# Kernel tuning notes

Hardware: AMD Instinct MI355X
Metric: run time of the kernel (lower is better)

Reference implementation:

```python
import jax, jax.numpy as jnp
import numpy as np

EPSILON = 10.0
N_ITERS = 10
TOL = 1e-06
N, DIM = 8192, 128


def setup_inputs() -> dict:
    key = jax.random.key(0)
    kx, ky = jax.random.split(key)
    x = jax.random.normal(kx, (N, DIM), dtype=jnp.float32)
    y = jax.random.normal(ky, (N, DIM), dtype=jnp.float32)
    return {"x": x, "y": y}


def _sinkhorn_plan(C):
    # uniform marginals, as in the torch module defaults
    n = C.shape[0]
    a = jnp.full((n,), 1.0 / n, dtype=C.dtype)
    b = a
    K = jnp.exp(-C / EPSILON)  # [n, n]
    u0 = jnp.ones((n,), dtype=C.dtype)
    v0 = jnp.ones((n,), dtype=C.dtype)

    def step(carry, _):
        u, v, done = carry
        u_new = a / (K @ v)
        v_new = b / (K.T @ u_new)
        # torch breaks AFTER applying the update, so the converging step is kept
        conv = jnp.linalg.norm(u_new - u) < TOL
        u = jnp.where(done, u, u_new)
        v = jnp.where(done, v, v_new)
        return (u, v, done | conv), None

    (u, v, _), _ = jax.lax.scan(step, (u0, v0, jnp.array(False)), None, length=N_ITERS)
    # diag(u) @ K @ diag(v) == u[:,None] * K * v[None,:] (no diag materialization)
    return u[:, None] * K * v[None, :]


def reference(x, y):
    # torch.cdist(x, y, p=2): pairwise L2 distances [n, n]
    x2 = jnp.sum(x * x, axis=1)
    y2 = jnp.sum(y * y, axis=1)
    d2 = x2[:, None] + y2[None, :] - 2.0 * (x @ y.T)
    C = jnp.sqrt(jnp.maximum(d2, 0.0))

    P = _sinkhorn_plan(C)
    transport_cost = jnp.sum(P * C)
    entropy = -jnp.sum(P * jnp.log(P + 1e-09))
    divergence = transport_cost + EPSILON * entropy
    return divergence, P
```

## Files before the change

kernel.cpp:

```cpp
#include <hip/hip_runtime.h>

#define N 8192
#define DIM 128
#define EPS 10.0f
#define AINV (1.0f / 8192.0f)
#define C1 (-0.14426950408889634f)
#define C1SQ (0.020813712f)

typedef __attribute__((ext_vector_type(8))) short short8;
typedef __attribute__((ext_vector_type(4))) float f32x4;

static __device__ __forceinline__ unsigned short f2bf(float f) {
  unsigned int b = __float_as_uint(f);
  unsigned int lsb = (b >> 16) & 1u;
  b += 0x7fffu + lsb;
  return (unsigned short)(b >> 16);
}

__global__ __launch_bounds__(256) void k_convert(const float* __restrict__ x, const float* __restrict__ y,
                                                 unsigned short* __restrict__ xb, unsigned short* __restrict__ yb,
                                                 float* __restrict__ x2, float* __restrict__ y2,
                                                 float* __restrict__ u, float* __restrict__ vpartB,
                                                 double* __restrict__ accs) {
  int r = blockIdx.x * 4 + (threadIdx.x >> 6);
  int l = threadIdx.x & 63;
  const float* src = (r < N) ? (x + (size_t)r * DIM) : (y + (size_t)(r - N) * DIM);
  float2 f = ((const float2*)src)[l];
  unsigned short* dst = (r < N) ? (xb + (size_t)r * DIM) : (yb + (size_t)(r - N) * DIM);
  ushort2 h; h.x = f2bf(f.x); h.y = f2bf(f.y);
  int di = (((l >> 2) ^ (r & 7)) << 2) | (l & 3);
  ((ushort2*)dst)[di] = h;
  float s = f.x * f.x + f.y * f.y;
#pragma unroll
  for (int off = 32; off >= 1; off >>= 1) s += __shfl_down(s, off);
  if (l == 0) { if (r < N) x2[r] = s; else y2[r - N] = s; }
  if (r < N) {
    if (l == 0) { u[r] = 1.f; vpartB[r] = AINV; }
    else if (l < 16) vpartB[(size_t)l * N + r] = 0.f;
  }
  if (r == 0 && l == 0) { accs[0] = 0.0; accs[1] = 0.0; }
}

__global__ __launch_bounds__(256, 3) void k_pass(const unsigned short* __restrict__ Ab,
                                                 const unsigned short* __restrict__ Bb,
                                                 const float* __restrict__ a2, const float* __restrict__ b2,
                                                 const float* __restrict__ wpart,
                                                 float* __restrict__ outpart,
                                                 float* __restrict__ u_arr,
                                                 int write_u) {
  __shared__ float wv_lds[1024];
  __shared__ float b2_lds[1024];
  const int jc = blockIdx.x;
  const int ic = blockIdx.y;
  const int i0 = ic * 128;
  const int tid = threadIdx.x;
  const int wid = tid >> 6, lane = tid & 63;
  const uint4* ag = (const uint4*)Ab + (size_t)i0 * 16;
  const uint4* bwin = (const uint4*)Bb + (size_t)jc * 1024 * 16;
  const int wr = (wid >> 1) * 64, wc = (wid & 1) * 32;
  const int lhi = lane >> 4, llo = lane & 15;
  short8 afr[4][4];
#pragma unroll
  for (int kk = 0; kk < 4; ++kk)
#pragma unroll
    for (int m = 0; m < 4; ++m) {
      int rx = wr + m * 16 + llo;
      afr[kk][m] = *(const short8*)(ag + rx * 16 + ((kk * 4 + lhi) ^ (rx & 7)));
    }
  float a2v[4][4], rsum[4][4];
#pragma unroll
  for (int m = 0; m < 4; ++m)
#pragma unroll
    for (int r = 0; r < 4; ++r) {
      a2v[m][r] = a2[i0 + wr + m * 16 + lhi * 4 + r] * C1SQ;
      rsum[m][r] = 0.f;
    }
  {
    const float4* wp4 = (const float4*)wpart;
    int w4 = jc * 256 + tid;
    float4 s4 = wp4[w4];
#pragma unroll
    for (int q = 1; q < 16; ++q) {
      float4 p = wp4[(size_t)q * 2048 + w4];
      s4.x += p.x; s4.y += p.y; s4.z += p.z; s4.w += p.w;
    }
    float4 wn;
    wn.x = AINV * __builtin_amdgcn_rcpf(s4.x);
    wn.y = AINV * __builtin_amdgcn_rcpf(s4.y);
    wn.z = AINV * __builtin_amdgcn_rcpf(s4.z);
    wn.w = AINV * __builtin_amdgcn_rcpf(s4.w);
    ((float4*)wv_lds)[tid] = wn;
    float4 b4 = ((const float4*)b2)[w4];
    b4.x *= C1SQ; b4.y *= C1SQ; b4.z *= C1SQ; b4.w *= C1SQ;
    ((float4*)b2_lds)[tid] = b4;
    if (write_u && ic == 0) ((float4*)u_arr)[w4] = wn;
  }
  __syncthreads();
  for (int sc = 0; sc < 16; ++sc) {
    float wv[2], b2v[2];
#pragma unroll
    for (int n = 0; n < 2; ++n) {
      int jl = sc * 64 + wc + n * 16 + llo;
      wv[n] = wv_lds[jl];
      b2v[n] = b2_lds[jl];
    }
    f32x4 acc[4][2];
    f32x4 zero = {0.f, 0.f, 0.f, 0.f};
#pragma unroll
    for (int m = 0; m < 4; ++m)
#pragma unroll
      for (int n = 0; n < 2; ++n) acc[m][n] = zero;
#pragma unroll
    for (int kk = 0; kk < 4; ++kk) {
      short8 bfr[2];
#pragma unroll
      for (int n = 0; n < 2; ++n) {
        int rw = sc * 64 + wc + n * 16 + llo;
        bfr[n] = *(const short8*)(bwin + (size_t)rw * 16 + ((kk * 4 + lhi) ^ (llo & 7)));
      }
#pragma unroll
      for (int m = 0; m < 4; ++m)
#pragma unroll
        for (int n = 0; n < 2; ++n)
          acc[m][n] = __builtin_amdgcn_mfma_f32_16x16x32_bf16(afr[kk][m], bfr[n], acc[m][n], 0, 0, 0);
    }
#pragma unroll
    for (int m = 0; m < 4; ++m)
#pragma unroll
      for (int n = 0; n < 2; ++n)
#pragma unroll
        for (int r = 0; r < 4; ++r) {
          float tt = fmaf(-2.f * C1SQ, acc[m][n][r], a2v[m][r] + b2v[n]);
          float ss = __builtin_amdgcn_sqrtf(fmaxf(tt, 0.f));
          rsum[m][r] = fmaf(__builtin_amdgcn_exp2f(-ss), wv[n], rsum[m][r]);
        }
  }
#pragma unroll
  for (int m = 0; m < 4; ++m)
#pragma unroll
    for (int r = 0; r < 4; ++r) {
      float s = rsum[m][r];
      s += __shfl_xor(s, 1);
      s += __shfl_xor(s, 2);
      s += __shfl_xor(s, 4);
      s += __shfl_xor(s, 8);
      rsum[m][r] = s;
    }
  if (llo == 0) {
    float* vp = outpart + (size_t)(jc * 2 + (wid & 1)) * N;
#pragma unroll
    for (int m = 0; m < 4; ++m)
#pragma unroll
      for (int r = 0; r < 4; ++r)
        vp[i0 + wr + m * 16 + lhi * 4 + r] = rsum[m][r];
  }
}

__global__ __launch_bounds__(256) void k_final(const unsigned short* __restrict__ xb,
                                               const unsigned short* __restrict__ yb,
                                               const float* __restrict__ x2, const float* __restrict__ y2,
                                               const float* __restrict__ u, const float* __restrict__ vpartB,
                                               float* __restrict__ D, double* __restrict__ accs) {
  __shared__ float vv_lds[128];
  __shared__ double r0[256], r1[256];
  const int bid = blockIdx.x;
  const int iy = (bid & 7) + ((bid >> 9) << 3);
  const int jx = (bid >> 3) & 63;
  const int i0 = iy * 128;
  const int j0 = jx * 128;
  const int tid = threadIdx.x;
  const uint4* xg = (const uint4*)xb + (size_t)i0 * 16;
  const uint4* yg = (const uint4*)yb + (size_t)j0 * 16;
  if (tid < 32) {
    const float4* vp4 = (const float4*)vpartB;
    int w4 = (j0 >> 2) + tid;
    float4 s4 = vp4[w4];
#pragma unroll
    for (int q = 1; q < 16; ++q) {
      float4 p = vp4[(size_t)q * 2048 + w4];
      s4.x += p.x; s4.y += p.y; s4.z += p.z; s4.w += p.w;
    }
    float4 vn;
    vn.x = AINV * __builtin_amdgcn_rcpf(s4.x);
    vn.y = AINV * __builtin_amdgcn_rcpf(s4.y);
    vn.z = AINV * __builtin_amdgcn_rcpf(s4.z);
    vn.w = AINV * __builtin_amdgcn_rcpf(s4.w);
    ((float4*)vv_lds)[tid] = vn;
  }
  __syncthreads();
  const int wid = tid >> 6, lane = tid & 63;
  const int wr = (wid >> 1) * 64, wc = (wid & 1) * 64;
  const int lhi = lane >> 4, llo = lane & 15;
  float x2v[4][4], uvv[4][4], y2v[4], vv[4];
#pragma unroll
  for (int m = 0; m < 4; ++m)
#pragma unroll
    for (int r = 0; r < 4; ++r) {
      int i = i0 + wr + m * 16 + lhi * 4 + r;
      x2v[m][r] = x2[i];
      uvv[m][r] = u[i];
    }
#pragma unroll
  for (int n = 0; n < 4; ++n) {
    int j = j0 + wc + n * 16 + llo;
    y2v[n] = y2[j];
    vv[n] = vv_lds[wc + n * 16 + llo];
  }
  f32x4 acc[4][4];
  f32x4 zero = {0.f, 0.f, 0.f, 0.f};
#pragma unroll
  for (int m = 0; m < 4; ++m)
#pragma unroll
    for (int n = 0; n < 4; ++n) acc[m][n] = zero;
#pragma unroll
  for (int kk = 0; kk < 4; ++kk) {
    short8 af[4], bfr[4];
#pragma unroll
    for (int m = 0; m < 4; ++m) {
      int rx = wr + m * 16 + llo;
      af[m] = *(const short8*)(xg + rx * 16 + ((kk * 4 + lhi) ^ (rx & 7)));
      int ry = wc + m * 16 + llo;
      bfr[m] = *(const short8*)(yg + ry * 16 + ((kk * 4 + lhi) ^ (ry & 7)));
    }
#pragma unroll
    for (int m = 0; m < 4; ++m)
#pragma unroll
      for (int n = 0; n < 4; ++n)
        acc[m][n] = __builtin_amdgcn_mfma_f32_16x16x32_bf16(af[m], bfr[n], acc[m][n], 0, 0, 0);
  }
  float lc = 0.f, le = 0.f;
#pragma unroll
  for (int m = 0; m < 4; ++m) {
#pragma unroll
    for (int n = 0; n < 4; ++n) {
#pragma unroll
      for (int r = 0; r < 4; ++r) {
        int i = i0 + wr + m * 16 + lhi * 4 + r;
        int j = j0 + wc + n * 16 + llo;
        float d2 = fmaf(-2.f, acc[m][n][r], x2v[m][r] + y2v[n]);
        float c = __builtin_amdgcn_sqrtf(fmaxf(d2, 0.f));
        float k = __builtin_amdgcn_exp2f(c * C1);
        float p = uvv[m][r] * k * vv[n];
        D[1 + (size_t)i * N + j] = p;
        lc = fmaf(p, c, lc);
        le = fmaf(p, __logf(p + 1e-9f), le);
      }
    }
  }
  r0[tid] = (double)lc;
  r1[tid] = (double)le;
  __syncthreads();
  for (int s = 128; s > 0; s >>= 1) {
    if (tid < s) {
      r0[tid] += r0[tid + s];
      r1[tid] += r1[tid + s];
    }
    __syncthreads();
  }
  if (tid == 0) {
    atomicAdd(&accs[0], r0[0]);
    atomicAdd(&accs[1], r1[0]);
  }
}

__global__ void k_write_div(float* D, const double* accs) {
  if (threadIdx.x == 0 && blockIdx.x == 0)
    D[0] = (float)(accs[0] - (double)EPS * accs[1]);
}

extern "C" void kernel_launch(void* const* d_in, const int* in_sizes, int n_in,
                              void* d_out, int out_size, void* d_ws, size_t ws_size,
                              hipStream_t stream) {
  const float* x = (const float*)d_in[0];
  const float* y = (const float*)d_in[1];
  float* D = (float*)d_out;
  char* w = (char*)d_ws;
  unsigned short* xb = (unsigned short*)w;
  unsigned short* yb = (unsigned short*)(w + 2097152);
  float* fb = (float*)(w + 4194304);
  float* x2 = fb;
  float* y2 = fb + 8192;
  float* u = fb + 16384;
  float* vpartA = fb + 24576;
  float* vpartB = vpartA + 16 * N;
  double* accs = (double*)(vpartB + 16 * N);

  k_convert<<<4096, 256, 0, stream>>>(x, y, xb, yb, x2, y2, u, vpartB, accs);
  k_pass<<<dim3(8, 64), 256, 0, stream>>>(xb, yb, x2, y2, vpartB, vpartA, u, 0);
  k_pass<<<dim3(8, 64), 256, 0, stream>>>(yb, xb, y2, x2, vpartA, vpartB, u, 0);
  k_pass<<<dim3(8, 64), 256, 0, stream>>>(xb, yb, x2, y2, vpartB, vpartA, u, 0);
  k_pass<<<dim3(8, 64), 256, 0, stream>>>(yb, xb, y2, x2, vpartA, vpartB, u, 1);
  k_final<<<4096, 256, 0, stream>>>(xb, yb, x2, y2, u, vpartB, D, accs);
  k_write_div<<<1, 64, 0, stream>>>(D, accs);
}
```

Baseline: 254.0 us.

## Store bf16 operands in MFMA fragment order and restructure final plan kernel

The convert kernel now writes bf16 x/y in a fragment-major layout (16-row groups, 64 lanes per k-chunk), so every MFMA operand load in the pass and final kernels becomes one contiguous 16-byte-per-lane read without XOR swizzle arithmetic. The final kernel is reorganised so each block handles 16 rows across half the columns, keeping the A fragments resident and streaming B. It also writes D in row-contiguous 16-wide segments. The v reconstruction from partial sums is moved into a small separate kernel that packs v with y2, which adds one extra launch.

```diff
diff --git a/kernel.cpp b/kernel.cpp
--- a/kernel.cpp
+++ b/kernel.cpp
@@ -26,10 +26,11 @@
   int l = threadIdx.x & 63;
   const float* src = (r < N) ? (x + (size_t)r * DIM) : (y + (size_t)(r - N) * DIM);
   float2 f = ((const float2*)src)[l];
-  unsigned short* dst = (r < N) ? (xb + (size_t)r * DIM) : (yb + (size_t)(r - N) * DIM);
+  unsigned short* dstbase = (r < N) ? xb : yb;
+  int rr = (r < N) ? r : r - N;
   ushort2 h; h.x = f2bf(f.x); h.y = f2bf(f.y);
-  int di = (((l >> 2) ^ (r & 7)) << 2) | (l & 3);
-  ((ushort2*)dst)[di] = h;
+  int idx2 = ((rr >> 4) << 10) + ((l >> 2) << 6) + ((rr & 15) << 2) + (l & 3);
+  ((ushort2*)dstbase)[idx2] = h;
   float s = f.x * f.x + f.y * f.y;
 #pragma unroll
   for (int off = 32; off >= 1; off >>= 1) s += __shfl_down(s, off);
@@ -55,18 +56,16 @@
   const int i0 = ic * 128;
   const int tid = threadIdx.x;
   const int wid = tid >> 6, lane = tid & 63;
-  const uint4* ag = (const uint4*)Ab + (size_t)i0 * 16;
-  const uint4* bwin = (const uint4*)Bb + (size_t)jc * 1024 * 16;
   const int wr = (wid >> 1) * 64, wc = (wid & 1) * 32;
   const int lhi = lane >> 4, llo = lane & 15;
+  const uint4* afrag = (const uint4*)Ab;
+  const uint4* bfrag = (const uint4*)Bb;
   short8 afr[4][4];
 #pragma unroll
   for (int kk = 0; kk < 4; ++kk)
 #pragma unroll
-    for (int m = 0; m < 4; ++m) {
-      int rx = wr + m * 16 + llo;
-      afr[kk][m] = *(const short8*)(ag + rx * 16 + ((kk * 4 + lhi) ^ (rx & 7)));
-    }
+    for (int m = 0; m < 4; ++m)
+      afr[kk][m] = *(const short8*)(afrag + ((ic * 8 + (wid >> 1) * 4 + m) * 256 + kk * 64 + lane));
   float a2v[4][4], rsum[4][4];
 #pragma unroll
   for (int m = 0; m < 4; ++m)
@@ -114,10 +113,8 @@
     for (int kk = 0; kk < 4; ++kk) {
       short8 bfr[2];
 #pragma unroll
-      for (int n = 0; n < 2; ++n) {
-        int rw = sc * 64 + wc + n * 16 + llo;
-        bfr[n] = *(const short8*)(bwin + (size_t)rw * 16 + ((kk * 4 + lhi) ^ (llo & 7)));
-      }
+      for (int n = 0; n < 2; ++n)
+        bfr[n] = *(const short8*)(bfrag + ((jc * 64 + sc * 4 + (wid & 1) * 2 + n) * 256 + kk * 64 + lane));
 #pragma unroll
       for (int m = 0; m < 4; ++m)
 #pragma unroll
@@ -156,96 +153,73 @@
   }
 }
 
+__global__ void k_vrecon(const float* __restrict__ vpartB, const float* __restrict__ y2,
+                         float2* __restrict__ vy2) {
+  int j = blockIdx.x * 256 + threadIdx.x;
+  float s = 0.f;
+#pragma unroll
+  for (int q = 0; q < 16; ++q) s += vpartB[(size_t)q * N + j];
+  float2 o; o.x = AINV * __builtin_amdgcn_rcpf(s); o.y = y2[j];
+  vy2[j] = o;
+}
+
 __global__ __launch_bounds__(256) void k_final(const unsigned short* __restrict__ xb,
                                                const unsigned short* __restrict__ yb,
-                                               const float* __restrict__ x2, const float* __restrict__ y2,
-                                               const float* __restrict__ u, const float* __restrict__ vpartB,
+                                               const float* __restrict__ x2,
+                                               const float* __restrict__ u, const float2* __restrict__ vy2,
                                                float* __restrict__ D, double* __restrict__ accs) {
-  __shared__ float vv_lds[128];
   __shared__ double r0[256], r1[256];
-  const int bid = blockIdx.x;
-  const int iy = (bid & 7) + ((bid >> 9) << 3);
-  const int jx = (bid >> 3) & 63;
-  const int i0 = iy * 128;
-  const int j0 = jx * 128;
+  const int b = blockIdx.x;
+  const int i0 = (b >> 1) * 16;
+  const int ch = (b & 1) * 4096;
   const int tid = threadIdx.x;
-  const uint4* xg = (const uint4*)xb + (size_t)i0 * 16;
-  const uint4* yg = (const uint4*)yb + (size_t)j0 * 16;
-  if (tid < 32) {
-    const float4* vp4 = (const float4*)vpartB;
-    int w4 = (j0 >> 2) + tid;
-    float4 s4 = vp4[w4];
-#pragma unroll
-    for (int q = 1; q < 16; ++q) {
-      float4 p = vp4[(size_t)q * 2048 + w4];
-      s4.x += p.x; s4.y += p.y; s4.z += p.z; s4.w += p.w;
-    }
-    float4 vn;
-    vn.x = AINV * __builtin_amdgcn_rcpf(s4.x);
-    vn.y = AINV * __builtin_amdgcn_rcpf(s4.y);
-    vn.z = AINV * __builtin_amdgcn_rcpf(s4.z);
-    vn.w = AINV * __builtin_amdgcn_rcpf(s4.w);
-    ((float4*)vv_lds)[tid] = vn;
-  }
-  __syncthreads();
   const int wid = tid >> 6, lane = tid & 63;
-  const int wr = (wid >> 1) * 64, wc = (wid & 1) * 64;
   const int lhi = lane >> 4, llo = lane & 15;
-  float x2v[4][4], uvv[4][4], y2v[4], vv[4];
-#pragma unroll
-  for (int m = 0; m < 4; ++m)
-#pragma unroll
-    for (int r = 0; r < 4; ++r) {
-      int i = i0 + wr + m * 16 + lhi * 4 + r;
-      x2v[m][r] = x2[i];
-      uvv[m][r] = u[i];
-    }
-#pragma unroll
-  for (int n = 0; n < 4; ++n) {
-    int j = j0 + wc + n * 16 + llo;
-    y2v[n] = y2[j];
-    vv[n] = vv_lds[wc + n * 16 + llo];
-  }
-  f32x4 acc[4][4];
-  f32x4 zero = {0.f, 0.f, 0.f, 0.f};
-#pragma unroll
-  for (int m = 0; m < 4; ++m)
-#pragma unroll
-    for (int n = 0; n < 4; ++n) acc[m][n] = zero;
-#pragma unroll
-  for (int kk = 0; kk < 4; ++kk) {
-    short8 af[4], bfr[4];
-#pragma unroll
-    for (int m = 0; m < 4; ++m) {
-      int rx = wr + m * 16 + llo;
-      af[m] = *(const short8*)(xg + rx * 16 + ((kk * 4 + lhi) ^ (rx & 7)));
-      int ry = wc + m * 16 + llo;
-      bfr[m] = *(const short8*)(yg + ry * 16 + ((kk * 4 + lhi) ^ (ry & 7)));
-    }
-#pragma unroll
-    for (int m = 0; m < 4; ++m)
-#pragma unroll
-      for (int n = 0; n < 4; ++n)
-        acc[m][n] = __builtin_amdgcn_mfma_f32_16x16x32_bf16(af[m], bfr[n], acc[m][n], 0, 0, 0);
+  const int wc = wid * 32;
+  const uint4* xfrag = (const uint4*)xb;
+  const uint4* yfrag = (const uint4*)yb;
+  short8 af[4];
+#pragma unroll
+  for (int kk = 0; kk < 4; ++kk)
+    af[kk] = *(const short8*)(xfrag + ((b >> 1) * 256 + kk * 64 + lane));
+  float x2v[4], uvv[4];
+#pragma unroll
+  for (int r = 0; r < 4; ++r) {
+    int i = i0 + lhi * 4 + r;
+    x2v[r] = x2[i];
+    uvv[r] = u[i];
   }
   float lc = 0.f, le = 0.f;
-#pragma unroll
-  for (int m = 0; m < 4; ++m) {
-#pragma unroll
-    for (int n = 0; n < 4; ++n) {
+  for (int sc = 0; sc < 32; ++sc) {
+    const int c0 = ch + sc * 128 + wc;
+    float2 vy[2];
+#pragma unroll
+    for (int n = 0; n < 2; ++n) vy[n] = vy2[c0 + n * 16 + llo];
+    f32x4 acc[2];
+    f32x4 zero = {0.f, 0.f, 0.f, 0.f};
+    acc[0] = zero; acc[1] = zero;
+#pragma unroll
+    for (int kk = 0; kk < 4; ++kk) {
+      short8 bfr[2];
+#pragma unroll
+      for (int n = 0; n < 2; ++n)
+        bfr[n] = *(const short8*)(yfrag + (((c0 + n * 16) >> 4) * 256 + kk * 64 + lane));
+#pragma unroll
+      for (int n = 0; n < 2; ++n)
+        acc[n] = __builtin_amdgcn_mfma_f32_16x16x32_bf16(af[kk], bfr[n], acc[n], 0, 0, 0);
+    }
+#pragma unroll
+    for (int n = 0; n < 2; ++n)
 #pragma unroll
       for (int r = 0; r < 4; ++r) {
-        int i = i0 + wr + m * 16 + lhi * 4 + r;
-        int j = j0 + wc + n * 16 + llo;
-        float d2 = fmaf(-2.f, acc[m][n][r], x2v[m][r] + y2v[n]);
+        float d2 = fmaf(-2.f, acc[n][r], x2v[r] + vy[n].y);
         float c = __builtin_amdgcn_sqrtf(fmaxf(d2, 0.f));
         float k = __builtin_amdgcn_exp2f(c * C1);
-        float p = uvv[m][r] * k * vv[n];
-        D[1 + (size_t)i * N + j] = p;
+        float p = uvv[r] * k * vy[n].x;
+        D[1 + (size_t)(i0 + lhi * 4 + r) * N + c0 + n * 16 + llo] = p;
         lc = fmaf(p, c, lc);
         le = fmaf(p, __logf(p + 1e-9f), le);
       }
-    }
   }
   r0[tid] = (double)lc;
   r1[tid] = (double)le;
@@ -283,13 +257,15 @@
   float* u = fb + 16384;
   float* vpartA = fb + 24576;
   float* vpartB = vpartA + 16 * N;
-  double* accs = (double*)(vpartB + 16 * N);
+  float2* vy2 = (float2*)(vpartB + 16 * N);
+  double* accs = (double*)(vy2 + N);
 
   k_convert<<<4096, 256, 0, stream>>>(x, y, xb, yb, x2, y2, u, vpartB, accs);
   k_pass<<<dim3(8, 64), 256, 0, stream>>>(xb, yb, x2, y2, vpartB, vpartA, u, 0);
   k_pass<<<dim3(8, 64), 256, 0, stream>>>(yb, xb, y2, x2, vpartA, vpartB, u, 0);
   k_pass<<<dim3(8, 64), 256, 0, stream>>>(xb, yb, x2, y2, vpartB, vpartA, u, 0);
   k_pass<<<dim3(8, 64), 256, 0, stream>>>(yb, xb, y2, x2, vpartA, vpartB, u, 1);
-  k_final<<<4096, 256, 0, stream>>>(xb, yb, x2, y2, u, vpartB, D, accs);
+  k_vrecon<<<32, 256, 0, stream>>>(vpartB, y2, vy2);
+  k_final<<<1024, 256, 0, stream>>>(xb, yb, x2, u, vy2, D, accs);
   k_write_div<<<1, 64, 0, stream>>>(D, accs);
 }
```

Result: faster. 225.8 us (-11.1%).
